# Performance work log

Hardware: AMD Instinct MI355X
Metric: run time of the kernel (lower is better)

## Reference

```python
import jax, jax.numpy as jnp
import numpy as np

B, C_IN, H, W = 32, 64, 64, 64
C_OUT = 128
KH, KW = 3, 3
PADDING = 2           # pad_l = 1, pad_r = 1 (replicate)
STRIDE = 1
TREE_DEPTH = 2
CONN_NUM = 1 << TREE_DEPTH          # 4
ACCL_SZ = C_IN * KH * KW            # 576


def setup_inputs() -> dict:
    key = jax.random.key(0)
    k1, k2, k3, k4 = jax.random.split(key, 4)
    x = jax.random.normal(k1, (B, C_IN, H, W), dtype=jnp.float32)
    weights = jax.random.normal(k2, (C_OUT, CONN_NUM), dtype=jnp.float32)
    bias = jax.random.normal(k3, (C_OUT, 1, 1), dtype=jnp.float32)
    conn_idx = jax.random.randint(k4, (C_OUT, CONN_NUM), 0, ACCL_SZ, dtype=jnp.int64 if jax.config.jax_enable_x64 else jnp.int32)
    return {"x": x, "weights": weights, "bias": bias, "conn_idx": conn_idx}


def reference(x, weights, bias, conn_idx):
    # Replicate-pad spatial dims (pad_l = PADDING//2, pad_r = PADDING - pad_l)
    pad_l = PADDING // 2
    pad_r = PADDING - pad_l
    x_pad = jnp.pad(x, ((0, 0), (0, 0), (pad_l, pad_r), (pad_l, pad_r)), mode="edge")
    Hp, Wp = x_pad.shape[2], x_pad.shape[3]
    Ho = (Hp - KH) // STRIDE + 1
    Wo = (Wp - KW) // STRIDE + 1

    # conn_idx flattens (c, i, j) with a = c*KH*KW + i*KW + j (matches torch
    # unfold(H).unfold(W) + permute + reshape layout). Decompose and gather
    # directly instead of the dense one-hot einsum (same math).
    c = conn_idx // (KH * KW)                 # [Co, N] channel
    rem = conn_idx % (KH * KW)
    di = rem // KW                            # [Co, N] row offset in kernel
    dj = rem % KW                             # [Co, N] col offset in kernel

    rows = di[:, :, None] + STRIDE * jnp.arange(Ho)   # [Co, N, Ho]
    cols = dj[:, :, None] + STRIDE * jnp.arange(Wo)   # [Co, N, Wo]

    # gathered[b, co, n, h, w] = x_pad[b, c[co,n], rows[co,n,h], cols[co,n,w]]
    gathered = x_pad[:, c[:, :, None, None], rows[:, :, :, None], cols[:, :, None, :]]
    # [B, Co, N, Ho, Wo]

    # Chebyshev (L-inf) "convolution": max over connections of |w - x|
    diff = jnp.abs(weights[None, :, :, None, None] - gathered)  # [B, Co, N, Ho, Wo]
    out = jnp.max(diff, axis=2) + bias[None]                    # [B, Co, Ho, Wo]
    return out
```

## Files before the change

### kernel.cpp

```cpp
#include <hip/hip_runtime.h>

#define BB     32
#define C_IN   64
#define HH     64
#define WW     64
#define C_OUT  128
#define CONN   4

__global__ __launch_bounds__(256) void lp_conv_bt_kernel(
    const float* __restrict__ x,
    const float* __restrict__ weights,
    const float* __restrict__ bias,
    const int*   __restrict__ conn,
    float*       __restrict__ out)
{
    const int bid = blockIdx.x;
    const int xcd = bid & 7;
    const int n   = bid >> 3;
    const int b   = (xcd << 2) | (n >> 8);
    const int o   = (n >> 1) & (C_OUT - 1);
    const int ihalf = n & 1;

    const int tid  = threadIdx.x;
    const int lane = tid & 63;
    int i0 = ihalf * 32 + (tid >> 6) * 8;
    i0 = __builtin_amdgcn_readfirstlane(i0);

    float acc[8];
#pragma unroll
    for (int i = 0; i < 8; ++i) acc[i] = 0.f;

#pragma unroll
    for (int k = 0; k < CONN; ++k) {
        const int   ci = conn[o * CONN + k];
        const float wk = weights[o * CONN + k];
        int c   = ci / 9;
        int rem = ci - c * 9;
        int di  = rem / 3;
        int dj  = rem - di * 3;

        int col = lane + dj - 1;
        col = min(max(col, 0), WW - 1);

        const float* base = x + (((size_t)b * C_IN + c) << 12);

#pragma unroll
        for (int i = 0; i < 8; ++i) {
            int hh = i0 + i + di - 1;
            hh = min(max(hh, 0), HH - 1);
            float v = base[(hh << 6) + col];
            acc[i] = fmaxf(acc[i], fabsf(wk - v));
        }
    }

    const float bo = bias[o];
    float* po = out + (((size_t)(b * C_OUT + o) * HH + i0) << 6) + lane;
#pragma unroll
    for (int i = 0; i < 8; ++i)
        __builtin_nontemporal_store(acc[i] + bo, po + (i << 6));
}

extern "C" void kernel_launch(void* const* d_in, const int* in_sizes, int n_in,
                              void* d_out, int out_size, void* d_ws, size_t ws_size,
                              hipStream_t stream) {
    const float* x       = (const float*)d_in[0];
    const float* weights = (const float*)d_in[1];
    const float* bias    = (const float*)d_in[2];
    const int*   conn    = (const int*)d_in[3];
    float*       out     = (float*)d_out;

    int grid = BB * C_OUT * 2;
    lp_conv_bt_kernel<<<grid, 256, 0, stream>>>(x, weights, bias, conn, out);
}
```

Measured before the change: 98.70 us.

## Vectorize loads and stores to float4 with shuffle-based column shifts

Each thread now handles four adjacent columns across four rows. It loads 16-byte float4 vectors and stores float4 results, replacing scalar 4-byte accesses. Horizontal kernel offsets are handled with a wave shuffle to fetch the neighbouring element, with edge replication at row boundaries. Each block now covers a full 64x64 output plane, so the grid is halved. This cuts the number of memory instructions and address calculations, but it adds shuffles and a data-dependent branch on dj, and leaves fewer, larger blocks.

Result: slower. 108.1 us (+9.5%).

```diff
diff --git a/kernel.cpp b/kernel.cpp
--- a/kernel.cpp
+++ b/kernel.cpp
@@ -6,6 +6,8 @@
 #define WW     64
 #define C_OUT  128
 #define CONN   4
+
+typedef float f32x4 __attribute__((ext_vector_type(4)));
 
 __global__ __launch_bounds__(256) void lp_conv_bt_kernel(
     const float* __restrict__ x,
@@ -17,18 +19,19 @@
     const int bid = blockIdx.x;
     const int xcd = bid & 7;
     const int n   = bid >> 3;
-    const int b   = (xcd << 2) | (n >> 8);
-    const int o   = (n >> 1) & (C_OUT - 1);
-    const int ihalf = n & 1;
+    const int b   = (xcd << 2) | (n >> 7);
+    const int o   = n & (C_OUT - 1);
 
     const int tid  = threadIdx.x;
     const int lane = tid & 63;
-    int i0 = ihalf * 32 + (tid >> 6) * 8;
+    const int q    = lane & 15;
+    const int r    = lane >> 4;
+    int i0 = (tid >> 6) << 4;
     i0 = __builtin_amdgcn_readfirstlane(i0);
 
-    float acc[8];
+    f32x4 acc[4];
 #pragma unroll
-    for (int i = 0; i < 8; ++i) acc[i] = 0.f;
+    for (int s = 0; s < 4; ++s) acc[s] = (f32x4)(0.f);
 
 #pragma unroll
     for (int k = 0; k < CONN; ++k) {
@@ -39,25 +42,56 @@
         int di  = rem / 3;
         int dj  = rem - di * 3;
 
-        int col = lane + dj - 1;
-        col = min(max(col, 0), WW - 1);
-
         const float* base = x + (((size_t)b * C_IN + c) << 12);
 
+        f32x4 v[4];
 #pragma unroll
-        for (int i = 0; i < 8; ++i) {
-            int hh = i0 + i + di - 1;
-            hh = min(max(hh, 0), HH - 1);
-            float v = base[(hh << 6) + col];
-            acc[i] = fmaxf(acc[i], fabsf(wk - v));
+        for (int s = 0; s < 4; ++s) {
+            int row = i0 + 4 * s + r + di - 1;
+            row = min(max(row, 0), HH - 1);
+            v[s] = *reinterpret_cast<const f32x4*>(base + (row << 6) + (q << 2));
+        }
+
+        if (dj == 0) {
+#pragma unroll
+            for (int s = 0; s < 4; ++s) {
+                float pw   = __shfl(v[s][3], lane - 1);
+                float left = (q == 0) ? v[s][0] : pw;
+                acc[s][0] = fmaxf(acc[s][0], fabsf(wk - left));
+                acc[s][1] = fmaxf(acc[s][1], fabsf(wk - v[s][0]));
+                acc[s][2] = fmaxf(acc[s][2], fabsf(wk - v[s][1]));
+                acc[s][3] = fmaxf(acc[s][3], fabsf(wk - v[s][2]));
+            }
+        } else if (dj == 1) {
+#pragma unroll
+            for (int s = 0; s < 4; ++s) {
+                acc[s][0] = fmaxf(acc[s][0], fabsf(wk - v[s][0]));
+                acc[s][1] = fmaxf(acc[s][1], fabsf(wk - v[s][1]));
+                acc[s][2] = fmaxf(acc[s][2], fabsf(wk - v[s][2]));
+                acc[s][3] = fmaxf(acc[s][3], fabsf(wk - v[s][3]));
+            }
+        } else {
+#pragma unroll
+            for (int s = 0; s < 4; ++s) {
+                float nx    = __shfl(v[s][0], lane + 1);
+                float right = (q == 15) ? v[s][3] : nx;
+                acc[s][0] = fmaxf(acc[s][0], fabsf(wk - v[s][1]));
+                acc[s][1] = fmaxf(acc[s][1], fabsf(wk - v[s][2]));
+                acc[s][2] = fmaxf(acc[s][2], fabsf(wk - v[s][3]));
+                acc[s][3] = fmaxf(acc[s][3], fabsf(wk - right));
+            }
         }
     }
 
     const float bo = bias[o];
-    float* po = out + (((size_t)(b * C_OUT + o) * HH + i0) << 6) + lane;
+    float* po = out + (((size_t)(b * C_OUT + o) * HH) << 6);
 #pragma unroll
-    for (int i = 0; i < 8; ++i)
-        __builtin_nontemporal_store(acc[i] + bo, po + (i << 6));
+    for (int s = 0; s < 4; ++s) {
+        int row = i0 + 4 * s + r;
+        f32x4 rv = acc[s] + bo;
+        __builtin_nontemporal_store(rv,
+            reinterpret_cast<f32x4*>(po + (row << 6) + (q << 2)));
+    }
 }
 
 extern "C" void kernel_launch(void* const* d_in, const int* in_sizes, int n_in,
@@ -69,6 +103,6 @@
     const int*   conn    = (const int*)d_in[3];
     float*       out     = (float*)d_out;
 
-    int grid = BB * C_OUT * 2;
+    int grid = BB * C_OUT;
     lp_conv_bt_kernel<<<grid, 256, 0, stream>>>(x, weights, bias, conn, out);
 }
```
